# Performance work log

Hardware: AMD Instinct MI355X
Metric: run time of the kernel (lower is better)

Reference implementation:

```python
import jax, jax.numpy as jnp
import numpy as np

D_MODEL = 2048
N_HEADS = 16
QK_HEAD_DIM = D_MODEL // N_HEADS  # 128
V_HEAD_DIM = 128
KV_LORA_RANK = 512
EPS = 1e-6
B, S = 2, 2048
ROPE_THETA = 10000.0


def setup_inputs() -> dict:
    key = jax.random.key(0)
    ks = jax.random.split(key, 7)
    x = jax.random.normal(ks[0], (B, S, D_MODEL), dtype=jnp.float32)
    # RoPE frequencies: freqs_cis[s, i] = exp(1j * s * theta^(-2i/d)) -> cos/sin
    inv_freq = 1.0 / (ROPE_THETA ** (np.arange(0, QK_HEAD_DIM, 2, dtype=np.float32) / QK_HEAD_DIM))
    ang = np.arange(S, dtype=np.float32)[:, None] * inv_freq[None, :]  # [S, 64]
    freqs_cos = jnp.asarray(np.cos(ang), dtype=jnp.float32)
    freqs_sin = jnp.asarray(np.sin(ang), dtype=jnp.float32)
    # Parameters stored as [in, out] so that y = x @ W
    def lin(k, fan_in, fan_out):
        return jax.random.normal(k, (fan_in, fan_out), dtype=jnp.float32) / np.sqrt(fan_in)
    w_kv_compress = lin(ks[1], D_MODEL, KV_LORA_RANK)
    kv_norm_w = jnp.ones((KV_LORA_RANK,), dtype=jnp.float32)
    w_k_up = lin(ks[2], KV_LORA_RANK, N_HEADS * QK_HEAD_DIM)
    w_v_up = lin(ks[3], KV_LORA_RANK, N_HEADS * V_HEAD_DIM)
    w_q = lin(ks[4], D_MODEL, N_HEADS * QK_HEAD_DIM)
    w_out = lin(ks[5], N_HEADS * V_HEAD_DIM, D_MODEL)
    return {"x": x, "freqs_cos": freqs_cos, "freqs_sin": freqs_sin,
            "w_kv_compress": w_kv_compress, "kv_norm_w": kv_norm_w,
            "w_k_up": w_k_up, "w_v_up": w_v_up, "w_q": w_q, "w_out": w_out}


def _rms_norm(x, w, eps=EPS):
    var = jnp.mean(jnp.square(x), axis=-1, keepdims=True)
    return x * jax.lax.rsqrt(var + eps) * w


def _apply_rope(t, cos, sin):
    # t: [B, S, H, D]; cos/sin: [S, D//2]; pairs are adjacent elements (complex view)
    b, s, h, d = t.shape
    tr = t.reshape(b, s, h, d // 2, 2)
    x1, x2 = tr[..., 0], tr[..., 1]
    c = cos[None, :, None, :]
    sn = sin[None, :, None, :]
    o1 = x1 * c - x2 * sn
    o2 = x1 * sn + x2 * c
    return jnp.stack([o1, o2], axis=-1).reshape(b, s, h, d)


def reference(x, freqs_cos, freqs_sin, w_kv_compress, kv_norm_w, w_k_up, w_v_up, w_q, w_out):
    b, s, _ = x.shape
    kv_latent = _rms_norm(x @ w_kv_compress, kv_norm_w)      # [B,S,R]
    k = (kv_latent @ w_k_up).reshape(b, s, N_HEADS, QK_HEAD_DIM)
    v = (kv_latent @ w_v_up).reshape(b, s, N_HEADS, V_HEAD_DIM)
    q = (x @ w_q).reshape(b, s, N_HEADS, QK_HEAD_DIM)
    q = _apply_rope(q, freqs_cos, freqs_sin)
    k = _apply_rope(k, freqs_cos, freqs_sin)
    scale = 1.0 / np.sqrt(QK_HEAD_DIM)
    scores = jnp.einsum('bqhd,bkhd->bhqk', q, k) * scale     # [B,H,S,S]
    causal = jnp.tril(jnp.ones((s, s), dtype=bool))
    scores = jnp.where(causal[None, None], scores, jnp.finfo(scores.dtype).min)
    probs = jax.nn.softmax(scores, axis=-1)
    attn = jnp.einsum('bhqk,bkhd->bqhd', probs, v)           # [B,S,H,Dv]
    out = attn.reshape(b, s, N_HEADS * V_HEAD_DIM) @ w_out   # [B,S,d_model]
    return out
```

## Files before the change

### kernel.cpp

```cpp
#include <hip/hip_runtime.h>

typedef unsigned short u16;
typedef __attribute__((ext_vector_type(8))) short bf16x8;
typedef __attribute__((ext_vector_type(4))) float floatx4;

__device__ __forceinline__ float bf2f(u16 h) {
  return __uint_as_float(((unsigned int)h) << 16);
}
__device__ __forceinline__ u16 f2bf(float f) {
  unsigned int u = __float_as_uint(f);
  u += 0x7fffu + ((u >> 16) & 1u);
  return (u16)(u >> 16);
}
__device__ __forceinline__ u16 f2bf_hu(float f) {
  return (u16)((__float_as_uint(f) + 0x8000u) >> 16);
}
__device__ __forceinline__ float exp2fast(float x) {
  float r;
  asm("v_exp_f32 %0, %1" : "=v"(r) : "v"(x));
  return r;
}
__device__ __forceinline__ bool is_f32(const u16* probe) { return probe[0] == 0; }

#define GLOAD_LDS16(gsrc, ldst)                                                        \
  __builtin_amdgcn_global_load_lds(                                                    \
      (const __attribute__((address_space(1))) unsigned int*)(gsrc),                   \
      (__attribute__((address_space(3))) unsigned int*)(ldst), 16, 0, 0)

__global__ __launch_bounds__(256) void cvt_to_bf16(const void* __restrict__ in,
                                                   u16* __restrict__ out, int n,
                                                   const u16* __restrict__ probe) {
  int i = (blockIdx.x * 256 + threadIdx.x) * 8;
  if (i >= n) return;
  if (is_f32(probe)) {
    const float* f = (const float*)in;
    uint4 o;
    o.x = (unsigned)f2bf(f[i + 0]) | ((unsigned)f2bf(f[i + 1]) << 16);
    o.y = (unsigned)f2bf(f[i + 2]) | ((unsigned)f2bf(f[i + 3]) << 16);
    o.z = (unsigned)f2bf(f[i + 4]) | ((unsigned)f2bf(f[i + 5]) << 16);
    o.w = (unsigned)f2bf(f[i + 6]) | ((unsigned)f2bf(f[i + 7]) << 16);
    *(uint4*)(out + i) = o;
  } else {
    *(uint4*)(out + i) = *(const uint4*)((const u16*)in + i);
  }
}

__global__ __launch_bounds__(256) void transpose_cvt(const void* __restrict__ in,
                                                     u16* __restrict__ out,
                                                     int R, int C,
                                                     const u16* __restrict__ probe) {
  __shared__ u16 tile[32][33];
  int bx = blockIdx.x * 32;
  int by = blockIdx.y * 32;
  int tx = threadIdx.x & 31, ty = threadIdx.x >> 5;
  if (is_f32(probe)) {
    const float* f = (const float*)in;
    for (int i = 0; i < 32; i += 8)
      tile[ty + i][tx] = f2bf(f[(size_t)(by + ty + i) * C + (bx + tx)]);
  } else {
    const u16* u = (const u16*)in;
    for (int i = 0; i < 32; i += 8)
      tile[ty + i][tx] = u[(size_t)(by + ty + i) * C + (bx + tx)];
  }
  __syncthreads();
  for (int i = 0; i < 32; i += 8)
    out[(size_t)(bx + ty + i) * R + (by + tx)] = tile[tx][ty + i];
}

__global__ __launch_bounds__(256) void gemm_bt(const u16* __restrict__ A,
                                               const u16* __restrict__ BT,
                                               void* __restrict__ C,
                                               int M, int N, int K,
                                               const u16* __restrict__ probe) {
  __shared__ __align__(16) u16 As[128 * 32];
  __shared__ __align__(16) u16 Bs[128 * 32];
  const int m0 = blockIdx.y * 128, n0 = blockIdx.x * 128;
  const int t = threadIdx.x;
  const int wave = t >> 6, lane = t & 63;
  const int wm = (wave >> 1) * 64, wn = (wave & 1) * 64;
  const int quad = lane >> 4, l16 = lane & 15;
  const bool f32o = is_f32(probe);
  floatx4 acc[4][4];
  for (int i = 0; i < 4; ++i)
    for (int j = 0; j < 4; ++j) acc[i][j] = (floatx4){0.f, 0.f, 0.f, 0.f};

  for (int kt = 0; kt < K; kt += 32) {
    __syncthreads();
    for (int i = 0; i < 2; ++i) {
      int e = (i * 256 + t) * 8;
      int r = e >> 5, c = e & 31;
      GLOAD_LDS16(A + (size_t)(m0 + r) * K + kt + c, As + e);
      GLOAD_LDS16(BT + (size_t)(n0 + r) * K + kt + c, Bs + e);
    }
    __syncthreads();
    bf16x8 af[4], bfr[4];
    for (int i = 0; i < 4; ++i)
      af[i] = *(const bf16x8*)&As[(wm + i * 16 + l16) * 32 + quad * 8];
    for (int j = 0; j < 4; ++j)
      bfr[j] = *(const bf16x8*)&Bs[(wn + j * 16 + l16) * 32 + quad * 8];
    for (int i = 0; i < 4; ++i)
      for (int j = 0; j < 4; ++j)
        acc[i][j] = __builtin_amdgcn_mfma_f32_16x16x32_bf16(af[i], bfr[j], acc[i][j], 0, 0, 0);
  }
  for (int i = 0; i < 4; ++i) {
    int rbase = m0 + wm + i * 16 + quad * 4;
    for (int j = 0; j < 4; ++j) {
      int col = n0 + wn + j * 16 + l16;
      if (f32o) {
        float* Cf = (float*)C;
        for (int r = 0; r < 4; ++r) Cf[(size_t)(rbase + r) * N + col] = acc[i][j][r];
      } else {
        u16* Ch = (u16*)C;
        for (int r = 0; r < 4; ++r) Ch[(size_t)(rbase + r) * N + col] = f2bf(acc[i][j][r]);
      }
    }
  }
}

__global__ __launch_bounds__(256) void gemm_fused(const u16* __restrict__ A,
                                                  const u16* __restrict__ BT,
                                                  u16* __restrict__ Ca, int sa,
                                                  u16* __restrict__ Cb, int sb,
                                                  int M, int N, int K, int nsplit,
                                                  int vmode,
                                                  const u16* __restrict__ fc,
                                                  const u16* __restrict__ fs,
                                                  float oscale) {
  __shared__ __align__(16) u16 As[128 * 32];
  __shared__ __align__(16) u16 Bs[128 * 32];
  const int m0 = blockIdx.y * 128, n0 = blockIdx.x * 128;
  const int t = threadIdx.x;
  const int wave = t >> 6, lane = t & 63;
  const int wm = (wave >> 1) * 64, wn = (wave & 1) * 64;
  const int quad = lane >> 4, l16 = lane & 15;
  floatx4 acc[4][4];
  for (int i = 0; i < 4; ++i)
    for (int j = 0; j < 4; ++j) acc[i][j] = (floatx4){0.f, 0.f, 0.f, 0.f};

  for (int kt = 0; kt < K; kt += 32) {
    __syncthreads();
    for (int i = 0; i < 2; ++i) {
      int e = (i * 256 + t) * 8;
      int r = e >> 5, c = e & 31;
      GLOAD_LDS16(A + (size_t)(m0 + r) * K + kt + c, As + e);
      GLOAD_LDS16(BT + (size_t)(n0 + r) * K + kt + c, Bs + e);
    }
    __syncthreads();
    bf16x8 af[4], bfr[4];
    for (int i = 0; i < 4; ++i)
      af[i] = *(const bf16x8*)&As[(wm + i * 16 + l16) * 32 + quad * 8];
    for (int j = 0; j < 4; ++j)
      bfr[j] = *(const bf16x8*)&Bs[(wn + j * 16 + l16) * 32 + quad * 8];
    for (int i = 0; i < 4; ++i)
      for (int j = 0; j < 4; ++j)
        acc[i][j] = __builtin_amdgcn_mfma_f32_16x16x32_bf16(af[i], bfr[j], acc[i][j], 0, 0, 0);
  }

  if (n0 < nsplit) {
    const bool odd = (l16 & 1);
    for (int i = 0; i < 4; ++i) {
      int rbase = m0 + wm + i * 16 + quad * 4;
      for (int j = 0; j < 4; ++j) {
        int col = n0 + wn + j * 16 + l16;
        int p = (wn + j * 16 + l16) >> 1;
        for (int r = 0; r < 4; ++r) {
          int srow = (rbase + r) & 2047;
          float c = bf2f(fc[srow * 64 + p]);
          float sn = bf2f(fs[srow * 64 + p]);
          float v = acc[i][j][r];
          float pv = __shfl_xor(v, 1);
          float o = fmaf(v, c, odd ? pv * sn : -pv * sn);
          Ca[(size_t)(rbase + r) * sa + col] = f2bf(o * oscale);
        }
      }
    }
  } else if (vmode == 0) {
    for (int i = 0; i < 4; ++i) {
      int rbase = m0 + wm + i * 16 + quad * 4;
      for (int j = 0; j < 4; ++j) {
        int col = n0 - nsplit + wn + j * 16 + l16;
        for (int r = 0; r < 4; ++r)
          Cb[(size_t)(rbase + r) * sb + col] = f2bf(acc[i][j][r]);
      }
    }
  } else {
    for (int i = 0; i < 4; ++i) {
      int token0 = m0 + wm + i * 16 + quad * 4;
      for (int j = 0; j < 4; ++j) {
        int ch = n0 - nsplit + wn + j * 16 + l16;
        size_t base = (((size_t)((token0 >> 11) * 16 + (ch >> 7)) * 128 + (ch & 127)) << 11) +
                      (token0 & 2047);
        ushort4 pk;
        pk.x = f2bf(acc[i][j][0]);
        pk.y = f2bf(acc[i][j][1]);
        pk.z = f2bf(acc[i][j][2]);
        pk.w = f2bf(acc[i][j][3]);
        *(ushort4*)(Cb + base) = pk;
      }
    }
  }
}

__global__ __launch_bounds__(256) void rmsnorm_kernel(u16* __restrict__ t,
                                                      const u16* __restrict__ w) {
  int row = blockIdx.x * 4 + (threadIdx.x >> 6);
  int lane = threadIdx.x & 63;
  u16* xr = t + (size_t)row * 512;
  float v[8];
  float ss = 0.f;
  for (int i = 0; i < 8; ++i) {
    v[i] = bf2f(xr[lane + i * 64]);
    ss += v[i] * v[i];
  }
  for (int d = 32; d > 0; d >>= 1) ss += __shfl_xor(ss, d);
  float r = rsqrtf(ss * (1.f / 512.f) + 1e-6f);
  for (int i = 0; i < 8; ++i) xr[lane + i * 64] = f2bf(v[i] * r * bf2f(w[lane + i * 64]));
}

__global__ __launch_bounds__(256) void attn_kernel(const u16* __restrict__ q,
                                                   const u16* __restrict__ k,
                                                   const u16* __restrict__ vt,
                                                   u16* __restrict__ o) {
  const int S = 2048;
  __shared__ __align__(16) u16 Kt[64 * 128];
  __shared__ __align__(16) u16 Vt[128 * 64];
  __shared__ __align__(16) u16 P[4][16][64];
  const int t = threadIdx.x;
  const int w = t >> 6, lane = t & 63;
  const int quad = lane >> 4, l16 = lane & 15;
  const int bh = blockIdx.x;
  const int b = bh >> 4, h = bh & 15;
  const int qb = (int)gridDim.y - 1 - (int)blockIdx.y;
  const int q0 = qb * 64 + w * 16;

  const u16* qbase = q + ((size_t)(b * S + q0 + l16)) * 2048 + h * 128;
  bf16x8 qf[4];
  for (int c = 0; c < 4; ++c) qf[c] = *(const bf16x8*)(qbase + c * 32 + quad * 8);

  const u16* kbase = k + (size_t)b * S * 2048 + h * 128;
  const u16* vtb = vt + (size_t)bh * 128 * S;

  const int ksrow = t >> 4, ksc = t & 15;
  const int vsrow = t >> 3, vsc = t & 7;

  bf16x8 onesf;
#pragma unroll
  for (int i = 0; i < 8; ++i) onesf[i] = (short)0x3F80;

  float m_i[4], l_i[4];
  floatx4 acc[8];
  for (int r = 0; r < 4; ++r) { m_i[r] = -1e30f; l_i[r] = 0.f; }
  for (int nd = 0; nd < 8; ++nd) acc[nd] = (floatx4){0.f, 0.f, 0.f, 0.f};

  const int kmax = q0 + 15;
  const int qbase64 = qb * 64;
  for (int kb = 0; kb <= qbase64; kb += 64) {
    const bool diag = (kb == qbase64);
    __syncthreads();
    for (int j = 0; j < 4; ++j) {
      int row = j * 16 + ksrow;
      GLOAD_LDS16(kbase + (size_t)(kb + row) * 2048 + (ksc ^ (row & 15)) * 8,
                  Kt + (size_t)(row * 16 + ksc) * 8);
    }
    for (int j = 0; j < 4; ++j) {
      int row = j * 32 + vsrow;
      GLOAD_LDS16(vtb + (size_t)row * S + kb + ((vsc ^ (row & 7)) * 8),
                  Vt + (size_t)(row * 8 + vsc) * 8);
    }
    __syncthreads();

    floatx4 s[4];
    if (!diag) {
      for (int ns = 0; ns < 4; ++ns) {
        s[ns] = (floatx4){0.f, 0.f, 0.f, 0.f};
        for (int c = 0; c < 4; ++c) {
          bf16x8 kf = *(const bf16x8*)&Kt[(ns * 16 + l16) * 128 + ((c * 4 + quad) ^ l16) * 8];
          s[ns] = __builtin_amdgcn_mfma_f32_16x16x32_bf16(qf[c], kf, s[ns], 0, 0, 0);
        }
      }
    } else {
      for (int ns = 0; ns < 4; ++ns) {
        if (kb + ns * 16 <= kmax) {
          s[ns] = (floatx4){0.f, 0.f, 0.f, 0.f};
          for (int c = 0; c < 4; ++c) {
            bf16x8 kf = *(const bf16x8*)&Kt[(ns * 16 + l16) * 128 + ((c * 4 + quad) ^ l16) * 8];
            s[ns] = __builtin_amdgcn_mfma_f32_16x16x32_bf16(qf[c], kf, s[ns], 0, 0, 0);
          }
          int key = kb + ns * 16 + l16;
          for (int r = 0; r < 4; ++r)
            s[ns][r] = (key > q0 + quad * 4 + r) ? -1e30f : s[ns][r];
        } else {
          s[ns] = (floatx4){-1e30f, -1e30f, -1e30f, -1e30f};
        }
      }
    }
    float tmax[4];
    for (int r = 0; r < 4; ++r) {
      float v = fmaxf(fmaxf(s[0][r], s[1][r]), fmaxf(s[2][r], s[3][r]));
      for (int d = 1; d < 16; d <<= 1) v = fmaxf(v, __shfl_xor(v, d));
      tmax[r] = v;
    }
    bool grow = (tmax[0] > m_i[0] + 8.f) || (tmax[1] > m_i[1] + 8.f) ||
                (tmax[2] > m_i[2] + 8.f) || (tmax[3] > m_i[3] + 8.f);
    if (__any(grow)) {
      for (int r = 0; r < 4; ++r) {
        float mn = fmaxf(m_i[r], tmax[r]);
        float alpha = exp2fast(m_i[r] - mn);
        m_i[r] = mn;
        l_i[r] *= alpha;
        for (int nd = 0; nd < 8; ++nd) acc[nd][r] *= alpha;
      }
    }
    for (int ns = 0; ns < 4; ++ns)
      for (int r = 0; r < 4; ++r) s[ns][r] = exp2fast(s[ns][r] - m_i[r]);
    for (int ns = 0; ns < 4; ++ns)
      for (int r = 0; r < 4; ++r) {
        int row = quad * 4 + r;
        P[w][row][(((ns * 2 + (l16 >> 3)) ^ (row & 7)) << 3) | (l16 & 7)] = f2bf_hu(s[ns][r]);
      }
    floatx4 ls = (floatx4){0.f, 0.f, 0.f, 0.f};
    for (int kc = 0; kc < 2; ++kc) {
      if (!diag || kb + kc * 32 <= kmax) {
        bf16x8 pa = *(const bf16x8*)&P[w][l16][((kc * 4 + quad) ^ (l16 & 7)) * 8];
        ls = __builtin_amdgcn_mfma_f32_16x16x32_bf16(pa, onesf, ls, 0, 0, 0);
        for (int nd = 0; nd < 8; ++nd) {
          int d = nd * 16 + l16;
          bf16x8 vf = *(const bf16x8*)&Vt[(d * 8 + ((kc * 4 + quad) ^ (d & 7))) * 8];
          acc[nd] = __builtin_amdgcn_mfma_f32_16x16x32_bf16(pa, vf, acc[nd], 0, 0, 0);
        }
      }
    }
    for (int r = 0; r < 4; ++r) l_i[r] += ls[r];
  }
  u16* ob = o + ((size_t)(b * S + q0 + quad * 4)) * 2048 + h * 128;
  for (int r = 0; r < 4; ++r) {
    float inv = 1.f / l_i[r];
    for (int nd = 0; nd < 8; ++nd)
      ob[(size_t)r * 2048 + nd * 16 + l16] = f2bf(acc[nd][r] * inv);
  }
}

extern "C" void kernel_launch(void* const* d_in, const int* in_sizes, int n_in,
                              void* d_out, int out_size, void* d_ws, size_t ws_size,
                              hipStream_t stream) {
  const void* x    = d_in[0];
  const void* fcos = d_in[1];
  const void* fsin = d_in[2];
  const void* wkv  = d_in[3];
  const void* wnr  = d_in[4];
  const void* wku  = d_in[5];
  const void* wvu  = d_in[6];
  const void* wq   = d_in[7];
  const void* wo   = d_in[8];
  const u16* probe = (const u16*)fcos;

  const size_t MB = 1u << 20;
  char* ws = (char*)d_ws;
  u16* xc    = (u16*)(ws);
  u16* vtb   = (u16*)(ws);
  u16* qb    = (u16*)(ws + 16 * MB);
  u16* kb    = (u16*)(ws + 32 * MB);
  u16* ab    = (u16*)(ws + 48 * MB);
  u16* lat   = (u16*)(ws + 64 * MB);
  u16* wqT   = (u16*)(ws + 68 * MB);
  u16* woT   = (u16*)(ws + 68 * MB);
  u16* wkvT  = (u16*)(ws + 76 * MB);
  u16* wkT   = (u16*)(ws + 78 * MB);
  u16* wvT   = (u16*)(ws + 80 * MB);
  u16* fcosc = (u16*)(ws + 82 * MB);
  u16* fsinc = (u16*)(ws + 82 * MB + 256 * 1024);
  u16* wnrc  = (u16*)(ws + 82 * MB + 512 * 1024);

  const float QSCALE = 0.08838834764831845f * 1.4426950408889634f;
  dim3 blk(256);
  cvt_to_bf16<<<dim3(4096), blk, 0, stream>>>(x, xc, 8388608, probe);
  cvt_to_bf16<<<dim3(64), blk, 0, stream>>>(fcos, fcosc, 131072, probe);
  cvt_to_bf16<<<dim3(64), blk, 0, stream>>>(fsin, fsinc, 131072, probe);
  cvt_to_bf16<<<dim3(1), blk, 0, stream>>>(wnr, wnrc, 512, probe);

  transpose_cvt<<<dim3(64, 64), blk, 0, stream>>>(wq, wqT, 2048, 2048, probe);
  transpose_cvt<<<dim3(16, 64), blk, 0, stream>>>(wkv, wkvT, 2048, 512, probe);

  gemm_fused<<<dim3(20, 32), blk, 0, stream>>>(xc, wqT, qb, 2048, lat, 512,
                                               4096, 2560, 2048, 2048, 0,
                                               fcosc, fsinc, QSCALE);
  rmsnorm_kernel<<<dim3(1024), blk, 0, stream>>>(lat, wnrc);

  transpose_cvt<<<dim3(64, 16), blk, 0, stream>>>(wku, wkT, 512, 2048, probe);
  transpose_cvt<<<dim3(64, 16), blk, 0, stream>>>(wvu, wvT, 512, 2048, probe);
  gemm_fused<<<dim3(32, 32), blk, 0, stream>>>(lat, wkT, kb, 2048, vtb, 0,
                                               4096, 4096, 512, 2048, 1,
                                               fcosc, fsinc, 1.0f);

  transpose_cvt<<<dim3(64, 64), blk, 0, stream>>>(wo, woT, 2048, 2048, probe);

  attn_kernel<<<dim3(32, 32), blk, 0, stream>>>(qb, kb, vtb, ab);

  gemm_bt<<<dim3(16, 32), blk, 0, stream>>>(ab, woT, d_out, 4096, 2048, 2048, probe);
}
```

Baseline: 394.4 us.

## Replace GEMMs with 256x256 tiled, multi-buffered, swizzled 8-wave MFMA kernel

Replaces both GEMM kernels with one unified gemm8 kernel. It uses 256x256 output tiles, 512 threads, 128KB of dynamic LDS double-buffering two 32-wide k-slabs, XOR-swizzled LDS layout to avoid bank conflicts, and prefetch of the next k-tiles interleaved with MFMA phases under manual barriers and priority hints. The goal is more data reuse per block, lower LDS conflict stalls, and overlap of global loads with compute in the three projection GEMMs. The larger tiles mean fewer blocks (160/256/128), which risks underfilling the 256 CUs and could cost occupancy.

```diff
diff --git a/kernel.cpp b/kernel.cpp
--- a/kernel.cpp
+++ b/kernel.cpp
@@ -67,138 +67,223 @@
     out[(size_t)(bx + ty + i) * R + (by + tx)] = tile[tx][ty + i];
 }
 
-__global__ __launch_bounds__(256) void gemm_bt(const u16* __restrict__ A,
-                                               const u16* __restrict__ BT,
-                                               void* __restrict__ C,
-                                               int M, int N, int K,
-                                               const u16* __restrict__ probe) {
-  __shared__ __align__(16) u16 As[128 * 32];
-  __shared__ __align__(16) u16 Bs[128 * 32];
-  const int m0 = blockIdx.y * 128, n0 = blockIdx.x * 128;
+__global__ __launch_bounds__(512, 2) void gemm8(const u16* __restrict__ A,
+                                                const u16* __restrict__ BT,
+                                                void* __restrict__ Ca, int sa,
+                                                u16* __restrict__ Cb, int sb,
+                                                int N, int K, int nsplit, int mode,
+                                                const u16* __restrict__ fc,
+                                                const u16* __restrict__ fs,
+                                                float oscale,
+                                                const u16* __restrict__ probe) {
+  extern __shared__ __align__(16) u16 ldsbuf[];
+  u16* const AsB = ldsbuf;
+  u16* const BsB = ldsbuf + 32768;
+#define ASLOT(b, k) (AsB + ((((b) << 1) | (k)) << 13))
+#define BSLOT(b, k) (BsB + ((((b) << 1) | (k)) << 13))
+
   const int t = threadIdx.x;
-  const int wave = t >> 6, lane = t & 63;
-  const int wm = (wave >> 1) * 64, wn = (wave & 1) * 64;
+  const int lane = t & 63, wid = t >> 6;
   const int quad = lane >> 4, l16 = lane & 15;
-  const bool f32o = is_f32(probe);
-  floatx4 acc[4][4];
-  for (int i = 0; i < 4; ++i)
+  const int wr = wid >> 2, wc = wid & 3;
+  const int m0 = blockIdx.y * 256, n0 = blockIdx.x * 256;
+  const int NT = K >> 6;
+
+  const u16* const Abase = A + (size_t)m0 * K;
+  const u16* const Bbase = BT + (size_t)n0 * K;
+
+  const int e0 = t, e1 = 512 + t;
+  const int r0 = e0 >> 2, r1 = e1 >> 2;
+  const int sg0 = (e0 & 3) ^ ((r0 & 3) ^ ((r0 >> 2) & 3));
+  const int sg1 = (e1 & 3) ^ ((r1 & 3) ^ ((r1 >> 2) & 3));
+  const u16* const sa0 = Abase + (size_t)r0 * K + sg0 * 8;
+  const u16* const sa1 = Abase + (size_t)r1 * K + sg1 * 8;
+  const u16* const sb0 = Bbase + (size_t)r0 * K + sg0 * 8;
+  const u16* const sb1 = Bbase + (size_t)r1 * K + sg1 * 8;
+#define STAGE_A(slot, kb)                      \
+  do {                                         \
+    GLOAD_LDS16(sa0 + (kb), (slot) + e0 * 8);  \
+    GLOAD_LDS16(sa1 + (kb), (slot) + e1 * 8);  \
+  } while (0)
+#define STAGE_B(slot, kb)                      \
+  do {                                         \
+    GLOAD_LDS16(sb0 + (kb), (slot) + e0 * 8);  \
+    GLOAD_LDS16(sb1 + (kb), (slot) + e1 * 8);  \
+  } while (0)
+
+  const int gofs = (quad ^ ((l16 & 3) ^ ((l16 >> 2) & 3))) * 8;
+#define FRAG(slot, row) (*(const bf16x8*)((slot) + (row) * 32 + gofs))
+
+#define SYNC_MID()                                          \
+  __builtin_amdgcn_s_barrier();                             \
+  asm volatile("s_waitcnt lgkmcnt(0)" ::: "memory");        \
+  __builtin_amdgcn_sched_barrier(0)
+
+  floatx4 acc[8][4];
+#pragma unroll
+  for (int i = 0; i < 8; ++i)
+#pragma unroll
     for (int j = 0; j < 4; ++j) acc[i][j] = (floatx4){0.f, 0.f, 0.f, 0.f};
 
-  for (int kt = 0; kt < K; kt += 32) {
-    __syncthreads();
-    for (int i = 0; i < 2; ++i) {
-      int e = (i * 256 + t) * 8;
-      int r = e >> 5, c = e & 31;
-      GLOAD_LDS16(A + (size_t)(m0 + r) * K + kt + c, As + e);
-      GLOAD_LDS16(BT + (size_t)(n0 + r) * K + kt + c, Bs + e);
-    }
-    __syncthreads();
-    bf16x8 af[4], bfr[4];
-    for (int i = 0; i < 4; ++i)
-      af[i] = *(const bf16x8*)&As[(wm + i * 16 + l16) * 32 + quad * 8];
-    for (int j = 0; j < 4; ++j)
-      bfr[j] = *(const bf16x8*)&Bs[(wn + j * 16 + l16) * 32 + quad * 8];
-    for (int i = 0; i < 4; ++i)
-      for (int j = 0; j < 4; ++j)
-        acc[i][j] = __builtin_amdgcn_mfma_f32_16x16x32_bf16(af[i], bfr[j], acc[i][j], 0, 0, 0);
-  }
-  for (int i = 0; i < 4; ++i) {
-    int rbase = m0 + wm + i * 16 + quad * 4;
-    for (int j = 0; j < 4; ++j) {
-      int col = n0 + wn + j * 16 + l16;
-      if (f32o) {
-        float* Cf = (float*)C;
-        for (int r = 0; r < 4; ++r) Cf[(size_t)(rbase + r) * N + col] = acc[i][j][r];
-      } else {
-        u16* Ch = (u16*)C;
-        for (int r = 0; r < 4; ++r) Ch[(size_t)(rbase + r) * N + col] = f2bf(acc[i][j][r]);
-      }
-    }
-  }
-}
-
-__global__ __launch_bounds__(256) void gemm_fused(const u16* __restrict__ A,
-                                                  const u16* __restrict__ BT,
-                                                  u16* __restrict__ Ca, int sa,
-                                                  u16* __restrict__ Cb, int sb,
-                                                  int M, int N, int K, int nsplit,
-                                                  int vmode,
-                                                  const u16* __restrict__ fc,
-                                                  const u16* __restrict__ fs,
-                                                  float oscale) {
-  __shared__ __align__(16) u16 As[128 * 32];
-  __shared__ __align__(16) u16 Bs[128 * 32];
-  const int m0 = blockIdx.y * 128, n0 = blockIdx.x * 128;
-  const int t = threadIdx.x;
-  const int wave = t >> 6, lane = t & 63;
-  const int wm = (wave >> 1) * 64, wn = (wave & 1) * 64;
-  const int quad = lane >> 4, l16 = lane & 15;
-  floatx4 acc[4][4];
-  for (int i = 0; i < 4; ++i)
-    for (int j = 0; j < 4; ++j) acc[i][j] = (floatx4){0.f, 0.f, 0.f, 0.f};
-
-  for (int kt = 0; kt < K; kt += 32) {
-    __syncthreads();
-    for (int i = 0; i < 2; ++i) {
-      int e = (i * 256 + t) * 8;
-      int r = e >> 5, c = e & 31;
-      GLOAD_LDS16(A + (size_t)(m0 + r) * K + kt + c, As + e);
-      GLOAD_LDS16(BT + (size_t)(n0 + r) * K + kt + c, Bs + e);
-    }
-    __syncthreads();
-    bf16x8 af[4], bfr[4];
-    for (int i = 0; i < 4; ++i)
-      af[i] = *(const bf16x8*)&As[(wm + i * 16 + l16) * 32 + quad * 8];
-    for (int j = 0; j < 4; ++j)
-      bfr[j] = *(const bf16x8*)&Bs[(wn + j * 16 + l16) * 32 + quad * 8];
-    for (int i = 0; i < 4; ++i)
-      for (int j = 0; j < 4; ++j)
-        acc[i][j] = __builtin_amdgcn_mfma_f32_16x16x32_bf16(af[i], bfr[j], acc[i][j], 0, 0, 0);
-  }
-
-  if (n0 < nsplit) {
+  STAGE_A(ASLOT(0, 0), 0);
+  STAGE_B(BSLOT(0, 0), 0);
+  STAGE_A(ASLOT(0, 1), 32);
+  STAGE_B(BSLOT(0, 1), 32);
+  STAGE_A(ASLOT(1, 0), 64);
+  STAGE_B(BSLOT(1, 0), 64);
+  asm volatile("s_waitcnt vmcnt(4)" ::: "memory");
+  __builtin_amdgcn_s_barrier();
+
+  bf16x8 af[4], bfr[4];
+  const int arow = wr * 128 + l16;
+  const int brow = wc * 64 + l16;
+
+#pragma unroll 1
+  for (int u = 0; u < NT; ++u) {
+    const int cur = u & 1, oth = cur ^ 1;
+    u16* const A0 = ASLOT(cur, 0);
+    u16* const A1 = ASLOT(cur, 1);
+    u16* const B0 = BSLOT(cur, 0);
+    u16* const B1 = BSLOT(cur, 1);
+    const bool s1 = (u + 1 < NT), s2 = (u + 2 < NT);
+    const int kb1 = (u + 1) << 6, kb2 = (u + 2) << 6;
+
+#pragma unroll
+    for (int mi = 0; mi < 4; ++mi) af[mi] = FRAG(A0, arow + mi * 16);
+#pragma unroll
+    for (int nj = 0; nj < 4; ++nj) bfr[nj] = FRAG(B0, brow + nj * 16);
+    if (s1) STAGE_A(ASLOT(oth, 1), kb1 + 32);
+    SYNC_MID();
+    __builtin_amdgcn_s_setprio(1);
+#pragma unroll
+    for (int mi = 0; mi < 4; ++mi)
+#pragma unroll
+      for (int nj = 0; nj < 4; ++nj)
+        acc[mi][nj] = __builtin_amdgcn_mfma_f32_16x16x32_bf16(af[mi], bfr[nj], acc[mi][nj], 0, 0, 0);
+    __builtin_amdgcn_s_setprio(0);
+    __builtin_amdgcn_sched_barrier(0);
+    __builtin_amdgcn_s_barrier();
+
+#pragma unroll
+    for (int mi = 0; mi < 4; ++mi) af[mi] = FRAG(A0, arow + 64 + mi * 16);
+    if (s1) STAGE_B(BSLOT(oth, 1), kb1 + 32);
+    SYNC_MID();
+    __builtin_amdgcn_s_setprio(1);
+#pragma unroll
+    for (int mi = 0; mi < 4; ++mi)
+#pragma unroll
+      for (int nj = 0; nj < 4; ++nj)
+        acc[mi + 4][nj] = __builtin_amdgcn_mfma_f32_16x16x32_bf16(af[mi], bfr[nj], acc[mi + 4][nj], 0, 0, 0);
+    __builtin_amdgcn_s_setprio(0);
+    __builtin_amdgcn_sched_barrier(0);
+    if (u == NT - 1) asm volatile("s_waitcnt vmcnt(0)" ::: "memory");
+    __builtin_amdgcn_s_barrier();
+
+#pragma unroll
+    for (int mi = 0; mi < 4; ++mi) af[mi] = FRAG(A1, arow + mi * 16);
+#pragma unroll
+    for (int nj = 0; nj < 4; ++nj) bfr[nj] = FRAG(B1, brow + nj * 16);
+    if (s2) STAGE_A(A0, kb2);
+    SYNC_MID();
+    __builtin_amdgcn_s_setprio(1);
+#pragma unroll
+    for (int mi = 0; mi < 4; ++mi)
+#pragma unroll
+      for (int nj = 0; nj < 4; ++nj)
+        acc[mi][nj] = __builtin_amdgcn_mfma_f32_16x16x32_bf16(af[mi], bfr[nj], acc[mi][nj], 0, 0, 0);
+    __builtin_amdgcn_s_setprio(0);
+    __builtin_amdgcn_sched_barrier(0);
+    __builtin_amdgcn_s_barrier();
+
+#pragma unroll
+    for (int mi = 0; mi < 4; ++mi) af[mi] = FRAG(A1, arow + 64 + mi * 16);
+    if (s2) STAGE_B(B0, kb2);
+    SYNC_MID();
+    __builtin_amdgcn_s_setprio(1);
+#pragma unroll
+    for (int mi = 0; mi < 4; ++mi)
+#pragma unroll
+      for (int nj = 0; nj < 4; ++nj)
+        acc[mi + 4][nj] = __builtin_amdgcn_mfma_f32_16x16x32_bf16(af[mi], bfr[nj], acc[mi + 4][nj], 0, 0, 0);
+    __builtin_amdgcn_s_setprio(0);
+    __builtin_amdgcn_sched_barrier(0);
+    asm volatile("s_waitcnt vmcnt(4)" ::: "memory");
+    __builtin_amdgcn_s_barrier();
+  }
+
+  if (mode == 0) {
+    const bool f32o = is_f32(probe);
+#pragma unroll
+    for (int mi = 0; mi < 8; ++mi) {
+      int rbase = m0 + wr * 128 + mi * 16 + quad * 4;
+#pragma unroll
+      for (int nj = 0; nj < 4; ++nj) {
+        int col = n0 + wc * 64 + nj * 16 + l16;
+        if (f32o) {
+          float* Cf = (float*)Ca;
+          for (int r = 0; r < 4; ++r) Cf[(size_t)(rbase + r) * sa + col] = acc[mi][nj][r];
+        } else {
+          u16* Ch = (u16*)Ca;
+          for (int r = 0; r < 4; ++r) Ch[(size_t)(rbase + r) * sa + col] = f2bf(acc[mi][nj][r]);
+        }
+      }
+    }
+  } else if (n0 < nsplit) {
     const bool odd = (l16 & 1);
-    for (int i = 0; i < 4; ++i) {
-      int rbase = m0 + wm + i * 16 + quad * 4;
-      for (int j = 0; j < 4; ++j) {
-        int col = n0 + wn + j * 16 + l16;
-        int p = (wn + j * 16 + l16) >> 1;
+    u16* Ch = (u16*)Ca;
+#pragma unroll
+    for (int mi = 0; mi < 8; ++mi) {
+      int rbase = m0 + wr * 128 + mi * 16 + quad * 4;
+#pragma unroll
+      for (int nj = 0; nj < 4; ++nj) {
+        int col = n0 + wc * 64 + nj * 16 + l16;
+        int p = (col & 127) >> 1;
         for (int r = 0; r < 4; ++r) {
           int srow = (rbase + r) & 2047;
           float c = bf2f(fc[srow * 64 + p]);
           float sn = bf2f(fs[srow * 64 + p]);
-          float v = acc[i][j][r];
+          float v = acc[mi][nj][r];
           float pv = __shfl_xor(v, 1);
           float o = fmaf(v, c, odd ? pv * sn : -pv * sn);
-          Ca[(size_t)(rbase + r) * sa + col] = f2bf(o * oscale);
+          Ch[(size_t)(rbase + r) * sa + col] = f2bf(o * oscale);
         }
       }
     }
-  } else if (vmode == 0) {
-    for (int i = 0; i < 4; ++i) {
-      int rbase = m0 + wm + i * 16 + quad * 4;
-      for (int j = 0; j < 4; ++j) {
-        int col = n0 - nsplit + wn + j * 16 + l16;
+  } else if (mode == 1) {
+#pragma unroll
+    for (int mi = 0; mi < 8; ++mi) {
+      int rbase = m0 + wr * 128 + mi * 16 + quad * 4;
+#pragma unroll
+      for (int nj = 0; nj < 4; ++nj) {
+        int col = n0 - nsplit + wc * 64 + nj * 16 + l16;
         for (int r = 0; r < 4; ++r)
-          Cb[(size_t)(rbase + r) * sb + col] = f2bf(acc[i][j][r]);
+          Cb[(size_t)(rbase + r) * sb + col] = f2bf(acc[mi][nj][r]);
       }
     }
   } else {
-    for (int i = 0; i < 4; ++i) {
-      int token0 = m0 + wm + i * 16 + quad * 4;
-      for (int j = 0; j < 4; ++j) {
-        int ch = n0 - nsplit + wn + j * 16 + l16;
+#pragma unroll
+    for (int mi = 0; mi < 8; ++mi) {
+      int token0 = m0 + wr * 128 + mi * 16 + quad * 4;
+#pragma unroll
+      for (int nj = 0; nj < 4; ++nj) {
+        int ch = n0 - nsplit + wc * 64 + nj * 16 + l16;
         size_t base = (((size_t)((token0 >> 11) * 16 + (ch >> 7)) * 128 + (ch & 127)) << 11) +
                       (token0 & 2047);
         ushort4 pk;
-        pk.x = f2bf(acc[i][j][0]);
-        pk.y = f2bf(acc[i][j][1]);
-        pk.z = f2bf(acc[i][j][2]);
-        pk.w = f2bf(acc[i][j][3]);
+        pk.x = f2bf(acc[mi][nj][0]);
+        pk.y = f2bf(acc[mi][nj][1]);
+        pk.z = f2bf(acc[mi][nj][2]);
+        pk.w = f2bf(acc[mi][nj][3]);
         *(ushort4*)(Cb + base) = pk;
       }
     }
   }
+#undef ASLOT
+#undef BSLOT
+#undef STAGE_A
+#undef STAGE_B
+#undef FRAG
+#undef SYNC_MID
 }
 
 __global__ __launch_bounds__(256) void rmsnorm_kernel(u16* __restrict__ t,
@@ -373,6 +458,10 @@
 
   const float QSCALE = 0.08838834764831845f * 1.4426950408889634f;
   dim3 blk(256);
+
+  hipFuncSetAttribute((const void*)gemm8, hipFuncAttributeMaxDynamicSharedMemorySize,
+                      131072);
+
   cvt_to_bf16<<<dim3(4096), blk, 0, stream>>>(x, xc, 8388608, probe);
   cvt_to_bf16<<<dim3(64), blk, 0, stream>>>(fcos, fcosc, 131072, probe);
   cvt_to_bf16<<<dim3(64), blk, 0, stream>>>(fsin, fsinc, 131072, probe);
@@ -381,20 +470,22 @@
   transpose_cvt<<<dim3(64, 64), blk, 0, stream>>>(wq, wqT, 2048, 2048, probe);
   transpose_cvt<<<dim3(16, 64), blk, 0, stream>>>(wkv, wkvT, 2048, 512, probe);
 
-  gemm_fused<<<dim3(20, 32), blk, 0, stream>>>(xc, wqT, qb, 2048, lat, 512,
-                                               4096, 2560, 2048, 2048, 0,
-                                               fcosc, fsinc, QSCALE);
+  gemm8<<<dim3(10, 16), dim3(512), 131072, stream>>>(xc, wqT, qb, 2048, lat, 512,
+                                                     2560, 2048, 2048, 1,
+                                                     fcosc, fsinc, QSCALE, probe);
   rmsnorm_kernel<<<dim3(1024), blk, 0, stream>>>(lat, wnrc);
 
   transpose_cvt<<<dim3(64, 16), blk, 0, stream>>>(wku, wkT, 512, 2048, probe);
   transpose_cvt<<<dim3(64, 16), blk, 0, stream>>>(wvu, wvT, 512, 2048, probe);
-  gemm_fused<<<dim3(32, 32), blk, 0, stream>>>(lat, wkT, kb, 2048, vtb, 0,
-                                               4096, 4096, 512, 2048, 1,
-                                               fcosc, fsinc, 1.0f);
+  gemm8<<<dim3(16, 16), dim3(512), 131072, stream>>>(lat, wkT, kb, 2048, vtb, 0,
+                                                     4096, 512, 2048, 2,
+                                                     fcosc, fsinc, 1.0f, probe);
 
   transpose_cvt<<<dim3(64, 64), blk, 0, stream>>>(wo, woT, 2048, 2048, probe);
 
   attn_kernel<<<dim3(32, 32), blk, 0, stream>>>(qb, kb, vtb, ab);
 
-  gemm_bt<<<dim3(16, 32), blk, 0, stream>>>(ab, woT, d_out, 4096, 2048, 2048, probe);
-}
+  gemm8<<<dim3(8, 16), dim3(512), 131072, stream>>>(ab, woT, d_out, 2048, nullptr, 0,
+                                                    2048, 2048, 0, 0,
+                                                    nullptr, nullptr, 1.0f, probe);
+}
```

Result: no change. 389.3 us (-1.3%).
